# Kernel optimization log

Hardware: AMD Instinct MI355X
Metric: run time of the kernel (lower is better)

Reference implementation:

```python
import jax, jax.numpy as jnp
import numpy as np

B, N, S, C, NS = 2, 20000, 1024, 256, 16
RADIUS, HMIN, HMAX = 0.05, -0.02, 0.04
NA, ND = 12, 4
EPS = 1e-5  # BatchNorm eps


def setup_inputs() -> dict:
    key = jax.random.key(0)
    ks = jax.random.split(key, 40)
    def rn(k, shape, scale=0.05):
        return jax.random.normal(k, shape, jnp.float32) * scale
    inp = {
        "xyz": jax.random.uniform(ks[0], (B, N, 3), jnp.float32),
        "new_xyz": jax.random.uniform(ks[1], (B, S, 3), jnp.float32),
        "view_rot": jax.random.normal(ks[2], (B, S, 3, 3), jnp.float32),
        "features": jax.random.normal(ks[3], (B, C, N), jnp.float32),
    }
    i = 4
    for li, (o, ci) in enumerate([(512, C + 3), (256, 512), (256, 256)], 1):
        inp[f"mlp{li}_w"] = rn(ks[i], (o, ci)); inp[f"mlp{li}_b"] = rn(ks[i + 1], (o,))
        inp[f"mlp{li}_g"] = jnp.ones((o,), jnp.float32) + rn(ks[i + 2], (o,), 0.01)
        inp[f"mlp{li}_be"] = rn(ks[i + 3], (o,)); i += 4
    for name in ("c1", "c2"):
        inp[f"{name}_w"] = rn(ks[i], (256, 256)); inp[f"{name}_b"] = rn(ks[i + 1], (256,))
        inp[f"{name}_g"] = jnp.ones((256,), jnp.float32) + rn(ks[i + 2], (256,), 0.01)
        inp[f"{name}_be"] = rn(ks[i + 3], (256,)); i += 4
    inp["c3_w"] = rn(ks[i], (NA * ND * 2, 256)); inp["c3_b"] = rn(ks[i + 1], (NA * ND * 2,))
    return inp


def _bn(x, g, be):  # eval-mode BatchNorm with running_mean=0, running_var=1
    return x * (g / jnp.sqrt(1.0 + EPS)) + be


def _forward(xyz, new_xyz, view_rot, features,
             mlp1_w, mlp1_b, mlp1_g, mlp1_be,
             mlp2_w, mlp2_b, mlp2_g, mlp2_be,
             mlp3_w, mlp3_b, mlp3_g, mlp3_be,
             c1_w, c1_b, c1_g, c1_be,
             c2_w, c2_b, c2_g, c2_be,
             c3_w, c3_b):
    # ---- cylinder query (CUDA kernel math: r = rot @ (p - c), cylinder axis = x) ----
    # computed per rotation row to keep intermediates at (B,S,N) each
    comp = []
    for i in range(3):
        rw = view_rot[:, :, i, :]  # (B,S,3)
        comp.append(jnp.einsum('bsj,bpj->bsp', rw, xyz) - jnp.sum(rw * new_xyz, -1)[..., None])
    xr, yr, zr = comp  # each (B,S,N)
    mask = (yr * yr + zr * zr < RADIUS * RADIUS) & (xr > HMIN) & (xr < HMAX)
    # first-NS valid indices per seed (ascending), pad with first valid (0 if none)
    vals = jnp.where(mask, jnp.arange(N, dtype=jnp.int32), N)  # (B,S,N)
    neg_top, _ = jax.lax.top_k(-vals, NS)
    idx = -neg_top  # (B,S,NS) ascending
    first = idx[..., :1]
    first = jnp.where(first >= N, 0, first)
    idx = jnp.where(idx >= N, first, idx)
    # ---- group ----
    b_ix = jnp.arange(B)[:, None, None]
    g_xyz = xyz[b_ix, idx]                                  # (B,S,NS,3)
    g_feat = jnp.transpose(features, (0, 2, 1))[b_ix, idx]  # (B,S,NS,C)
    diff = (g_xyz - new_xyz[:, :, None, :]) / RADIUS        # normalize_xyz
    rot_xyz = jnp.einsum('bsnk,bskj->bsnj', diff, view_rot)  # rotate_xyz: diff @ rot
    h = jnp.concatenate([rot_xyz, g_feat], axis=-1)          # (B,S,NS,C+3)
    # ---- SharedMLP (1x1 conv2d + BN + ReLU) ----
    for w, bb, g, be in ((mlp1_w, mlp1_b, mlp1_g, mlp1_be),
                         (mlp2_w, mlp2_b, mlp2_g, mlp2_be),
                         (mlp3_w, mlp3_b, mlp3_g, mlp3_be)):
        h = jax.nn.relu(_bn(jnp.einsum('bsnc,oc->bsno', h, w) + bb, g, be))
    h = h.max(axis=2)  # max-pool over samples -> (B,S,256)
    # ---- pointwise conv1d head ----
    h = jax.nn.relu(_bn(jnp.einsum('bsc,oc->bso', h, c1_w) + c1_b, c1_g, c1_be))
    h = jax.nn.relu(_bn(jnp.einsum('bsc,oc->bso', h, c2_w) + c2_b, c2_g, c2_be))
    out = jnp.einsum('bsc,oc->bso', h, c3_w) + c3_b  # (B,S,NA*ND*2)
    return out


def reference(xyz, new_xyz, view_rot, features,
              mlp1_w, mlp1_b, mlp1_g, mlp1_be,
              mlp2_w, mlp2_b, mlp2_g, mlp2_be,
              mlp3_w, mlp3_b, mlp3_g, mlp3_be,
              c1_w, c1_b, c1_g, c1_be,
              c2_w, c2_b, c2_g, c2_be,
              c3_w, c3_b):
    return _forward(xyz, new_xyz, view_rot, features,
                    mlp1_w, mlp1_b, mlp1_g, mlp1_be,
                    mlp2_w, mlp2_b, mlp2_g, mlp2_be,
                    mlp3_w, mlp3_b, mlp3_g, mlp3_be,
                    c1_w, c1_b, c1_g, c1_be,
                    c2_w, c2_b, c2_g, c2_be,
                    c3_w, c3_b)
```

## Files before the change

kernel.cpp:

```cpp
#include <hip/hip_runtime.h>
#include <hip/hip_bf16.h>
#include <stdint.h>

#define B_   2
#define N_   20000
#define S_   1024
#define C_   256
#define NS_  16
#define NQ   (B_ * S_)
#define M_   (NQ * NS_)
#define K1P  288
#define O1   512
#define O2   256
#define O3   256
#define OUTC 96

#define R2C   ((float)(0.05 * 0.05))
#define HMINC ((float)(-0.02))
#define HMAXC ((float)(0.04))

__device__ __forceinline__ unsigned short f2b(float f) {
    union { float f; unsigned int i; } x; x.f = f;
    unsigned int r = x.i + 0x7FFFu + ((x.i >> 16) & 1u);
    return (unsigned short)(r >> 16);
}
__device__ __forceinline__ float b2f(unsigned short u) {
    union { unsigned int i; float f; } x; x.i = ((unsigned int)u) << 16; return x.f;
}

__global__ __launch_bounds__(256) void prep_w123(const float* __restrict__ m1w,
                                                 const float* __restrict__ m2w,
                                                 const float* __restrict__ m3w,
                                                 unsigned short* __restrict__ w1p,
                                                 unsigned short* __restrict__ w2p,
                                                 unsigned short* __restrict__ w3p) {
    int i = blockIdx.x * 256 + threadIdx.x;
    if (i < O1 * K1P) {
        int o = i / K1P, k = i - o * K1P;
        float v = 0.0f;
        if (k < 256)      v = m1w[o * 259 + 3 + k];
        else if (k < 259) v = m1w[o * 259 + (k - 256)];
        w1p[i] = (k < 259) ? f2b(v) : (unsigned short)0;
    } else if (i < O1 * K1P + O2 * 512) {
        int j = i - O1 * K1P;
        w2p[j] = f2b(m2w[j]);
    } else if (i < O1 * K1P + O2 * 512 + O3 * 256) {
        int j = i - O1 * K1P - O2 * 512;
        w3p[j] = f2b(m3w[j]);
    }
}

__global__ __launch_bounds__(256) void prep_head_w(const float* __restrict__ c1w,
                                                   const float* __restrict__ c2w,
                                                   const float* __restrict__ c3w,
                                                   unsigned short* __restrict__ c1wb,
                                                   unsigned short* __restrict__ c2wb,
                                                   unsigned short* __restrict__ c3wb) {
    int i = blockIdx.x * 256 + threadIdx.x;
    if (i < 65536) {
        c1wb[i] = f2b(c1w[i]);
    } else if (i < 131072) {
        c2wb[i - 65536] = f2b(c2w[i - 65536]);
    } else if (i < 163840) {
        int j = i - 131072;
        int o = j >> 8, k = j & 255;
        c3wb[j] = (o < OUTC) ? f2b(c3w[o * 256 + k]) : (unsigned short)0;
    }
}

__global__ __launch_bounds__(256) void transpose_feat(const float* __restrict__ feat,
                                                      unsigned short* __restrict__ feat_t) {
    __shared__ float tile[32][33];
    int n0 = blockIdx.x * 32, c0 = blockIdx.y * 32, b = blockIdx.z;
    int t = threadIdx.x;
    int nl = t & 31;
#pragma unroll
    for (int i = 0; i < 4; ++i) {
        int cl = (t >> 5) + i * 8;
        tile[cl][nl] = feat[((size_t)(b * C_ + c0 + cl)) * N_ + n0 + nl];
    }
    __syncthreads();
    int nr = t >> 3, c4 = (t & 7) * 4;
    ushort4 v;
    v.x = f2b(tile[c4 + 0][nr]);
    v.y = f2b(tile[c4 + 1][nr]);
    v.z = f2b(tile[c4 + 2][nr]);
    v.w = f2b(tile[c4 + 3][nr]);
    *(ushort4*)(feat_t + ((size_t)(b * N_ + n0 + nr)) * C_ + c0 + c4) = v;
}

__global__ __launch_bounds__(256) void cyl_query(const float* __restrict__ xyz,
                                                 const float* __restrict__ new_xyz,
                                                 const float* __restrict__ view_rot,
                                                 int* __restrict__ idx_out) {
#pragma clang fp contract(off)
    int q = blockIdx.x;
    int b = q >> 10;
    int t = threadIdx.x;
    int w = t >> 6, lane = t & 63;

    __shared__ int lists[4][NS_];
    __shared__ int cnts[4];

    const float* nq = new_xyz + (size_t)q * 3;
    float qx = nq[0], qy = nq[1], qz = nq[2];
    const float* rp = view_rot + (size_t)q * 9;
    float R[9];
#pragma unroll
    for (int i = 0; i < 9; ++i) R[i] = rp[i];
    float dq0 = (R[0]*qx + R[1]*qy) + R[2]*qz;
    float dq1 = (R[3]*qx + R[4]*qy) + R[5]*qz;
    float dq2 = (R[6]*qx + R[7]*qy) + R[8]*qz;

    int start = w * 5000;
    int end   = min(N_, start + 5000);
    int cnt = 0;
    const float* xb = xyz + (size_t)b * N_ * 3;

    for (int base = start; base < end && cnt < NS_; base += 64) {
        int p = base + lane;
        bool m = false;
        if (p < end) {
            const float* pp = xb + (size_t)p * 3;
            float px = pp[0], py = pp[1], pz = pp[2];
            float xr = ((R[0]*px + R[1]*py) + R[2]*pz) - dq0;
            float yr = ((R[3]*px + R[4]*py) + R[5]*pz) - dq1;
            float zr = ((R[6]*px + R[7]*py) + R[8]*pz) - dq2;
            m = ((yr*yr + zr*zr) < R2C) && (xr > HMINC) && (xr < HMAXC);
        }
        unsigned long long bal = __ballot(m);
        int below = __popcll(bal & ((1ull << lane) - 1ull));
        if (m) {
            int pos = cnt + below;
            if (pos < NS_) lists[w][pos] = p;
        }
        cnt += (int)__popcll(bal);
        if (cnt > NS_) cnt = NS_;
    }
    if (lane == 0) cnts[w] = cnt;
    __syncthreads();

    if (t == 0) {
        int buf[NS_]; int total = 0;
        for (int ww = 0; ww < 4 && total < NS_; ++ww)
            for (int i = 0; i < cnts[ww] && total < NS_; ++i)
                buf[total++] = lists[ww][i];
        int first = (total > 0) ? buf[0] : 0;
        for (int i = 0; i < NS_; ++i)
            idx_out[q * NS_ + i] = (i < total) ? buf[i] : first;
    }
}

__global__ __launch_bounds__(256) void build_h0(const float* __restrict__ xyz,
                                                const float* __restrict__ new_xyz,
                                                const float* __restrict__ view_rot,
                                                const unsigned short* __restrict__ feat_t,
                                                const int* __restrict__ idxs,
                                                unsigned short* __restrict__ h0) {
#pragma clang fp contract(off)
    int q = blockIdx.x;
    int b = q >> 10;
    int t = threadIdx.x;
    __shared__ int pidx[NS_];
    if (t < NS_) pidx[t] = idxs[q * NS_ + t];
    __syncthreads();

#pragma unroll
    for (int pass = 0; pass < 2; ++pass) {
        int n = pass * 8 + (t >> 5);
        int p = pidx[n];
        uint4 v = *(const uint4*)(feat_t + ((size_t)(b * N_ + p)) * C_ + (t & 31) * 8);
        *(uint4*)(h0 + (size_t)(q * NS_ + n) * K1P + (t & 31) * 8) = v;
    }

    if (t < NS_) {
        int n = t, p = pidx[n];
        const float* pp = xyz + ((size_t)b * N_ + p) * 3;
        const float* nq = new_xyz + (size_t)q * 3;
        float dx = (pp[0] - nq[0]) / 0.05f;
        float dy = (pp[1] - nq[1]) / 0.05f;
        float dz = (pp[2] - nq[2]) / 0.05f;
        const float* rp = view_rot + (size_t)q * 9;
        float r0 = (dx * rp[0] + dy * rp[3]) + dz * rp[6];
        float r1 = (dx * rp[1] + dy * rp[4]) + dz * rp[7];
        float r2 = (dx * rp[2] + dy * rp[5]) + dz * rp[8];
        size_t row = (size_t)(q * NS_ + n) * K1P;
        h0[row + 256] = f2b(r0);
        h0[row + 257] = f2b(r1);
        h0[row + 258] = f2b(r2);
    }
    for (int e = t; e < NS_ * 29; e += 256) {
        int n = e / 29, c = 259 + (e - n * 29);
        h0[(size_t)(q * NS_ + n) * K1P + c] = 0;
    }
}

typedef float f32x4 __attribute__((ext_vector_type(4)));
typedef short s16x8 __attribute__((ext_vector_type(8)));

__global__ __launch_bounds__(256) void gemm_bn_relu(const unsigned short* __restrict__ A,
                                                    const unsigned short* __restrict__ W,
                                                    const float* __restrict__ bias,
                                                    const float* __restrict__ gam,
                                                    const float* __restrict__ bet,
                                                    unsigned short* __restrict__ out,
                                                    int M, int Nn, int K) {
    __shared__ __align__(16) unsigned short As[128 * 32];
    __shared__ __align__(16) unsigned short Bs[128 * 32];
    int tid  = threadIdx.x;
    int lane = tid & 63, wave = tid >> 6;
    int m0 = blockIdx.x * 128, n0 = blockIdx.y * 128;
    int wm = (wave >> 1) * 64, wn = (wave & 1) * 64;

    f32x4 acc[4][4] = {};

    for (int k0 = 0; k0 < K; k0 += 32) {
        __syncthreads();
#pragma unroll
        for (int j = 0; j < 2; ++j) {
            int e = j * 256 + tid;
            int r = e >> 2, c8 = (e & 3) << 3;
            *(uint4*)&As[e * 8] = *(const uint4*)(A + (size_t)(m0 + r) * K + k0 + c8);
            *(uint4*)&Bs[e * 8] = *(const uint4*)(W + (size_t)(n0 + r) * K + k0 + c8);
        }
        __syncthreads();

        int kq = (lane >> 4) * 8, rr = lane & 15;
        s16x8 af[4], bfr[4];
#pragma unroll
        for (int i = 0; i < 4; ++i) af[i]  = *(const s16x8*)&As[(wm + i * 16 + rr) * 32 + kq];
#pragma unroll
        for (int j = 0; j < 4; ++j) bfr[j] = *(const s16x8*)&Bs[(wn + j * 16 + rr) * 32 + kq];
#pragma unroll
        for (int i = 0; i < 4; ++i)
#pragma unroll
            for (int j = 0; j < 4; ++j)
                acc[i][j] = __builtin_amdgcn_mfma_f32_16x16x32_bf16(af[i], bfr[j], acc[i][j], 0, 0, 0);
    }

    float inv = 1.0f / sqrtf(1.0f + 1e-5f);
    int col = lane & 15, rq = (lane >> 4) * 4;
#pragma unroll
    for (int j = 0; j < 4; ++j) {
        int n = n0 + wn + j * 16 + col;
        float sc = gam[n] * inv;
        float tb = bias[n] * sc + bet[n];
#pragma unroll
        for (int i = 0; i < 4; ++i) {
            int mbase = m0 + wm + i * 16 + rq;
#pragma unroll
            for (int r = 0; r < 4; ++r) {
                float v = acc[i][j][r] * sc + tb;
                v = fmaxf(v, 0.0f);
                out[(size_t)(mbase + r) * Nn + n] = f2b(v);
            }
        }
    }
}

__global__ __launch_bounds__(256) void gemm_bn_relu_maxpool(const unsigned short* __restrict__ A,
                                                            const unsigned short* __restrict__ W,
                                                            const float* __restrict__ bias,
                                                            const float* __restrict__ gam,
                                                            const float* __restrict__ bet,
                                                            unsigned short* __restrict__ hp,
                                                            int M, int Nn, int K) {
    __shared__ __align__(16) unsigned short As[128 * 32];
    __shared__ __align__(16) unsigned short Bs[128 * 32];
    int tid  = threadIdx.x;
    int lane = tid & 63, wave = tid >> 6;
    int m0 = blockIdx.x * 128, n0 = blockIdx.y * 128;
    int wm = (wave >> 1) * 64, wn = (wave & 1) * 64;

    f32x4 acc[4][4] = {};

    for (int k0 = 0; k0 < K; k0 += 32) {
        __syncthreads();
#pragma unroll
        for (int j = 0; j < 2; ++j) {
            int e = j * 256 + tid;
            int r = e >> 2, c8 = (e & 3) << 3;
            *(uint4*)&As[e * 8] = *(const uint4*)(A + (size_t)(m0 + r) * K + k0 + c8);
            *(uint4*)&Bs[e * 8] = *(const uint4*)(W + (size_t)(n0 + r) * K + k0 + c8);
        }
        __syncthreads();

        int kq = (lane >> 4) * 8, rr = lane & 15;
        s16x8 af[4], bfr[4];
#pragma unroll
        for (int i = 0; i < 4; ++i) af[i]  = *(const s16x8*)&As[(wm + i * 16 + rr) * 32 + kq];
#pragma unroll
        for (int j = 0; j < 4; ++j) bfr[j] = *(const s16x8*)&Bs[(wn + j * 16 + rr) * 32 + kq];
#pragma unroll
        for (int i = 0; i < 4; ++i)
#pragma unroll
            for (int j = 0; j < 4; ++j)
                acc[i][j] = __builtin_amdgcn_mfma_f32_16x16x32_bf16(af[i], bfr[j], acc[i][j], 0, 0, 0);
    }

    float inv = 1.0f / sqrtf(1.0f + 1e-5f);
    int col = lane & 15;
    int qbase = (m0 + wm) >> 4;
#pragma unroll
    for (int j = 0; j < 4; ++j) {
        int n = n0 + wn + j * 16 + col;
        float sc = gam[n] * inv;
        float tb = bias[n] * sc + bet[n];
#pragma unroll
        for (int i = 0; i < 4; ++i) {
            float mx = 0.0f;
#pragma unroll
            for (int r = 0; r < 4; ++r)
                mx = fmaxf(mx, acc[i][j][r] * sc + tb);
            mx = fmaxf(mx, __shfl_xor(mx, 16, 64));
            mx = fmaxf(mx, __shfl_xor(mx, 32, 64));
            if (lane < 16)
                hp[(size_t)(qbase + i) * Nn + n] = f2b(mx);
        }
    }
}

__global__ __launch_bounds__(256) void gemm_c3(const unsigned short* __restrict__ A,
                                               const unsigned short* __restrict__ W,
                                               const float* __restrict__ bias,
                                               float* __restrict__ out,
                                               int M, int K) {
    __shared__ __align__(16) unsigned short As[128 * 32];
    __shared__ __align__(16) unsigned short Bs[128 * 32];
    int tid  = threadIdx.x;
    int lane = tid & 63, wave = tid >> 6;
    int m0 = blockIdx.x * 128;
    int wm = (wave >> 1) * 64, wn = (wave & 1) * 64;

    f32x4 acc[4][4] = {};

    for (int k0 = 0; k0 < K; k0 += 32) {
        __syncthreads();
#pragma unroll
        for (int j = 0; j < 2; ++j) {
            int e = j * 256 + tid;
            int r = e >> 2, c8 = (e & 3) << 3;
            *(uint4*)&As[e * 8] = *(const uint4*)(A + (size_t)(m0 + r) * K + k0 + c8);
            *(uint4*)&Bs[e * 8] = *(const uint4*)(W + (size_t)r * K + k0 + c8);
        }
        __syncthreads();

        int kq = (lane >> 4) * 8, rr = lane & 15;
        s16x8 af[4], bfr[4];
#pragma unroll
        for (int i = 0; i < 4; ++i) af[i]  = *(const s16x8*)&As[(wm + i * 16 + rr) * 32 + kq];
#pragma unroll
        for (int j = 0; j < 4; ++j) bfr[j] = *(const s16x8*)&Bs[(wn + j * 16 + rr) * 32 + kq];
#pragma unroll
        for (int i = 0; i < 4; ++i)
#pragma unroll
            for (int j = 0; j < 4; ++j)
                acc[i][j] = __builtin_amdgcn_mfma_f32_16x16x32_bf16(af[i], bfr[j], acc[i][j], 0, 0, 0);
    }

    int col = lane & 15, rq = (lane >> 4) * 4;
#pragma unroll
    for (int j = 0; j < 4; ++j) {
        int n = wn + j * 16 + col;
        if (n >= OUTC) continue;
        float bb = bias[n];
#pragma unroll
        for (int i = 0; i < 4; ++i) {
            int mbase = m0 + wm + i * 16 + rq;
#pragma unroll
            for (int r = 0; r < 4; ++r)
                out[(size_t)(mbase + r) * OUTC + n] = acc[i][j][r] + bb;
        }
    }
}

extern "C" void kernel_launch(void* const* d_in, const int* in_sizes, int n_in,
                              void* d_out, int out_size, void* d_ws, size_t ws_size,
                              hipStream_t stream) {
    const float* xyz      = (const float*)d_in[0];
    const float* new_xyz  = (const float*)d_in[1];
    const float* view_rot = (const float*)d_in[2];
    const float* feat     = (const float*)d_in[3];
    const float* m1w = (const float*)d_in[4];
    const float* m1b = (const float*)d_in[5];
    const float* m1g = (const float*)d_in[6];
    const float* m1be= (const float*)d_in[7];
    const float* m2w = (const float*)d_in[8];
    const float* m2b = (const float*)d_in[9];
    const float* m2g = (const float*)d_in[10];
    const float* m2be= (const float*)d_in[11];
    const float* m3w = (const float*)d_in[12];
    const float* m3b = (const float*)d_in[13];
    const float* m3g = (const float*)d_in[14];
    const float* m3be= (const float*)d_in[15];
    const float* c1w = (const float*)d_in[16];
    const float* c1b = (const float*)d_in[17];
    const float* c1g = (const float*)d_in[18];
    const float* c1be= (const float*)d_in[19];
    const float* c2w = (const float*)d_in[20];
    const float* c2b = (const float*)d_in[21];
    const float* c2g = (const float*)d_in[22];
    const float* c2be= (const float*)d_in[23];
    const float* c3w = (const float*)d_in[24];
    const float* c3b = (const float*)d_in[25];

    char* ws = (char*)d_ws;
    int*            idxs = (int*)ws;
    unsigned short* w1p  = (unsigned short*)(ws + 131072);
    unsigned short* w2p  = (unsigned short*)(ws + 425984);
    unsigned short* w3p  = (unsigned short*)(ws + 688128);
    unsigned short* h0   = (unsigned short*)(ws + 819200);
    char*           h1b  = ws + 19693568;
    unsigned short* h1   = (unsigned short*)h1b;
    unsigned short* h2   = h0;
    unsigned short* featt= (unsigned short*)(h1b + 12582912);
    unsigned short* hp   = (unsigned short*)(h1b + 0);
    unsigned short* g1   = (unsigned short*)(h1b + 4194304);
    unsigned short* g2   = (unsigned short*)(h1b + 8388608);
    unsigned short* c1wb = (unsigned short*)(h1b + 12582912);
    unsigned short* c2wb = (unsigned short*)(h1b + 13631488);
    unsigned short* c3wb = (unsigned short*)(h1b + 14680064);

    hipLaunchKernelGGL(prep_w123, dim3((O1 * K1P + O2 * 512 + O3 * 256) / 256), dim3(256), 0, stream,
                       m1w, m2w, m3w, w1p, w2p, w3p);
    hipLaunchKernelGGL(cyl_query, dim3(NQ), dim3(256), 0, stream, xyz, new_xyz, view_rot, idxs);
    hipLaunchKernelGGL(transpose_feat, dim3(N_ / 32, C_ / 32, B_), dim3(256), 0, stream, feat, featt);
    hipLaunchKernelGGL(build_h0, dim3(NQ), dim3(256), 0, stream, xyz, new_xyz, view_rot, featt, idxs, h0);
    hipLaunchKernelGGL(gemm_bn_relu, dim3(M_ / 128, O1 / 128), dim3(256), 0, stream,
                       h0, w1p, m1b, m1g, m1be, h1, M_, O1, K1P);
    hipLaunchKernelGGL(gemm_bn_relu, dim3(M_ / 128, O2 / 128), dim3(256), 0, stream,
                       h1, w2p, m2b, m2g, m2be, h2, M_, O2, 512);
    hipLaunchKernelGGL(prep_head_w, dim3(163840 / 256), dim3(256), 0, stream,
                       c1w, c2w, c3w, c1wb, c2wb, c3wb);
    hipLaunchKernelGGL(gemm_bn_relu_maxpool, dim3(M_ / 128, O3 / 128), dim3(256), 0, stream,
                       h2, w3p, m3b, m3g, m3be, hp, M_, O3, 256);
    hipLaunchKernelGGL(gemm_bn_relu, dim3(NQ / 128, 256 / 128), dim3(256), 0, stream,
                       hp, c1wb, c1b, c1g, c1be, g1, NQ, 256, 256);
    hipLaunchKernelGGL(gemm_bn_relu, dim3(NQ / 128, 256 / 128), dim3(256), 0, stream,
                       g1, c2wb, c2b, c2g, c2be, g2, NQ, 256, 256);
    hipLaunchKernelGGL(gemm_c3, dim3(NQ / 128), dim3(256), 0, stream,
                       g2, c3wb, c3b, (float*)d_out, NQ, 256);
}
```

Measured before the change: 266.0 us.

## Replace brute-force cylinder query with uniform grid spatial hashing

Points are bucketed into a 16^3 uniform grid per batch using count, scan and scatter kernels. Each query then scans only the cells overlapping a conservative bounding box of its cylinder, computed from the inverse rotation. Candidates are kept in a per-wave shared buffer, and a wave-level selection picks the 16 smallest indices, which preserves the reference ordering. This is meant to cut the O(N) scan per query, at the cost of four extra small launches and atomics. The saving shrinks if the inverse rotations make the boxes large.

```diff
diff --git a/kernel.cpp b/kernel.cpp
--- a/kernel.cpp
+++ b/kernel.cpp
@@ -1,6 +1,7 @@
 #include <hip/hip_runtime.h>
 #include <hip/hip_bf16.h>
 #include <stdint.h>
+#include <limits.h>
 
 #define B_   2
 #define N_   20000
@@ -18,6 +19,11 @@
 #define R2C   ((float)(0.05 * 0.05))
 #define HMINC ((float)(-0.02))
 #define HMAXC ((float)(0.04))
+
+#define GDIM   16
+#define GCELLS (GDIM * GDIM * GDIM)
+#define GTOT   (B_ * GCELLS)
+#define CAP    256
 
 __device__ __forceinline__ unsigned short f2b(float f) {
     union { float f; unsigned int i; } x; x.f = f;
@@ -89,18 +95,112 @@
     *(ushort4*)(feat_t + ((size_t)(b * N_ + n0 + nr)) * C_ + c0 + c4) = v;
 }
 
-__global__ __launch_bounds__(256) void cyl_query(const float* __restrict__ xyz,
-                                                 const float* __restrict__ new_xyz,
-                                                 const float* __restrict__ view_rot,
-                                                 int* __restrict__ idx_out) {
+__global__ __launch_bounds__(256) void grid_zero(int* __restrict__ c) {
+    c[blockIdx.x * 256 + threadIdx.x] = 0;
+}
+
+__device__ __forceinline__ int cell_of(float px, float py, float pz, int b) {
+    int cx = (int)(px * (float)GDIM); cx = min(GDIM - 1, max(0, cx));
+    int cy = (int)(py * (float)GDIM); cy = min(GDIM - 1, max(0, cy));
+    int cz = (int)(pz * (float)GDIM); cz = min(GDIM - 1, max(0, cz));
+    return b * GCELLS + cz * (GDIM * GDIM) + cy * GDIM + cx;
+}
+
+__global__ __launch_bounds__(256) void grid_count(const float* __restrict__ xyz,
+                                                  int* __restrict__ counts) {
+    int i = blockIdx.x * 256 + threadIdx.x;
+    if (i < B_ * N_) {
+        int b = i / N_;
+        const float* p = xyz + (size_t)i * 3;
+        atomicAdd(counts + cell_of(p[0], p[1], p[2], b), 1);
+    }
+}
+
+__global__ __launch_bounds__(256) void grid_scan(const int* __restrict__ counts,
+                                                 int* __restrict__ start,
+                                                 int* __restrict__ cursor) {
+    __shared__ int part[256];
+    int t = threadIdx.x;
+    int local[32];
+    int s = 0;
+#pragma unroll
+    for (int i = 0; i < 32; ++i) { local[i] = counts[t * 32 + i]; s += local[i]; }
+    part[t] = s;
+    __syncthreads();
+    if (t == 0) {
+        int r = 0;
+        for (int i = 0; i < 256; ++i) { int x = part[i]; part[i] = r; r += x; }
+    }
+    __syncthreads();
+    int r = part[t];
+#pragma unroll
+    for (int i = 0; i < 32; ++i) {
+        start[t * 32 + i] = r;
+        cursor[t * 32 + i] = r;
+        r += local[i];
+    }
+    if (t == 255) start[GTOT] = r;
+}
+
+__global__ __launch_bounds__(256) void grid_scatter(const float* __restrict__ xyz,
+                                                    int* __restrict__ cursor,
+                                                    float4* __restrict__ sorted) {
+    int i = blockIdx.x * 256 + threadIdx.x;
+    if (i < B_ * N_) {
+        int b = i / N_, n = i - b * N_;
+        const float* p = xyz + (size_t)i * 3;
+        float px = p[0], py = p[1], pz = p[2];
+        int pos = atomicAdd(cursor + cell_of(px, py, pz, b), 1);
+        sorted[pos] = make_float4(px, py, pz, __int_as_float(n));
+    }
+}
+
+__device__ __forceinline__ void sort16(int* buf, int cnt, int lane) {
+    asm volatile("s_waitcnt lgkmcnt(0)" ::: "memory");
+    __builtin_amdgcn_sched_barrier(0);
+    int a0 = INT_MAX, a1 = INT_MAX, a2 = INT_MAX, a3 = INT_MAX;
+    if (lane < cnt)       a0 = buf[lane];
+    if (lane + 64 < cnt)  a1 = buf[lane + 64];
+    if (lane + 128 < cnt) a2 = buf[lane + 128];
+    if (lane + 192 < cnt) a3 = buf[lane + 192];
+#pragma unroll
+    for (int t = 0; t < NS_; ++t) {
+        int v = a0, sl = 0;
+        if (a1 < v) { v = a1; sl = 1; }
+        if (a2 < v) { v = a2; sl = 2; }
+        if (a3 < v) { v = a3; sl = 3; }
+        int pp = (sl << 6) | lane;
+#pragma unroll
+        for (int off = 1; off < 64; off <<= 1) {
+            int ov = __shfl_xor(v, off);
+            int op = __shfl_xor(pp, off);
+            if (ov < v) { v = ov; pp = op; }
+        }
+        if ((pp & 63) == lane) {
+            int s = pp >> 6;
+            if (s == 0) a0 = INT_MAX;
+            else if (s == 1) a1 = INT_MAX;
+            else if (s == 2) a2 = INT_MAX;
+            else a3 = INT_MAX;
+        }
+        if (lane == 0) buf[t] = v;
+    }
+    asm volatile("s_waitcnt lgkmcnt(0)" ::: "memory");
+    __builtin_amdgcn_sched_barrier(0);
+}
+
+__global__ __launch_bounds__(256) void cyl_query_grid(const float* __restrict__ new_xyz,
+                                                      const float* __restrict__ view_rot,
+                                                      const float4* __restrict__ sorted,
+                                                      const int* __restrict__ cell_start,
+                                                      int* __restrict__ idx_out) {
 #pragma clang fp contract(off)
-    int q = blockIdx.x;
+    int w = threadIdx.x >> 6, lane = threadIdx.x & 63;
+    int q = blockIdx.x * 4 + w;
     int b = q >> 10;
-    int t = threadIdx.x;
-    int w = t >> 6, lane = t & 63;
-
-    __shared__ int lists[4][NS_];
-    __shared__ int cnts[4];
+
+    __shared__ int bufs[4][CAP];
+    int* buf = bufs[w];
 
     const float* nq = new_xyz + (size_t)q * 3;
     float qx = nq[0], qy = nq[1], qz = nq[2];
@@ -112,42 +212,76 @@
     float dq1 = (R[3]*qx + R[4]*qy) + R[5]*qz;
     float dq2 = (R[6]*qx + R[7]*qy) + R[8]*qz;
 
-    int start = w * 5000;
-    int end   = min(N_, start + 5000);
-    int cnt = 0;
-    const float* xb = xyz + (size_t)b * N_ * 3;
-
-    for (int base = start; base < end && cnt < NS_; base += 64) {
-        int p = base + lane;
-        bool m = false;
-        if (p < end) {
-            const float* pp = xb + (size_t)p * 3;
-            float px = pp[0], py = pp[1], pz = pp[2];
-            float xr = ((R[0]*px + R[1]*py) + R[2]*pz) - dq0;
-            float yr = ((R[3]*px + R[4]*py) + R[5]*pz) - dq1;
-            float zr = ((R[6]*px + R[7]*py) + R[8]*pz) - dq2;
-            m = ((yr*yr + zr*zr) < R2C) && (xr > HMINC) && (xr < HMAXC);
-        }
-        unsigned long long bal = __ballot(m);
-        int below = __popcll(bal & ((1ull << lane) - 1ull));
-        if (m) {
-            int pos = cnt + below;
-            if (pos < NS_) lists[w][pos] = p;
-        }
-        cnt += (int)__popcll(bal);
-        if (cnt > NS_) cnt = NS_;
-    }
-    if (lane == 0) cnts[w] = cnt;
-    __syncthreads();
-
-    if (t == 0) {
-        int buf[NS_]; int total = 0;
-        for (int ww = 0; ww < 4 && total < NS_; ++ww)
-            for (int i = 0; i < cnts[ww] && total < NS_; ++i)
-                buf[total++] = lists[ww][i];
-        int first = (total > 0) ? buf[0] : 0;
-        for (int i = 0; i < NS_; ++i)
-            idx_out[q * NS_ + i] = (i < total) ? buf[i] : first;
+    int x0 = 0, x1 = GDIM - 1, y0 = 0, y1 = GDIM - 1, z0 = 0, z1 = GDIM - 1;
+    {
+        float det = R[0]*(R[4]*R[8]-R[5]*R[7])
+                  - R[1]*(R[3]*R[8]-R[5]*R[6])
+                  + R[2]*(R[3]*R[7]-R[4]*R[6]);
+        float adet = fabsf(det);
+        if (adet > 1e-30f) {
+            float id = 1.0f / det;
+            float m00 = (R[4]*R[8]-R[5]*R[7])*id, m01 = (R[2]*R[7]-R[1]*R[8])*id, m02 = (R[1]*R[5]-R[2]*R[4])*id;
+            float m10 = (R[5]*R[6]-R[3]*R[8])*id, m11 = (R[0]*R[8]-R[2]*R[6])*id, m12 = (R[2]*R[3]-R[0]*R[5])*id;
+            float m20 = (R[3]*R[7]-R[4]*R[6])*id, m21 = (R[1]*R[6]-R[0]*R[7])*id, m22 = (R[0]*R[4]-R[1]*R[3])*id;
+            const float mid = 0.5f * (HMINC + HMAXC);
+            const float hh  = 0.5f * (HMAXC - HMINC);
+            float cx = qx + m00 * mid, cy = qy + m10 * mid, cz = qz + m20 * mid;
+            float ex = hh * fabsf(m00) + 0.05f * sqrtf(m01*m01 + m02*m02);
+            float ey = hh * fabsf(m10) + 0.05f * sqrtf(m11*m11 + m12*m12);
+            float ez = hh * fabsf(m20) + 0.05f * sqrtf(m21*m21 + m22*m22);
+            ex = ex * 1.002f + 1e-3f;
+            ey = ey * 1.002f + 1e-3f;
+            ez = ez * 1.002f + 1e-3f;
+            x0 = (int)fmaxf(0.0f, fminf((float)(GDIM - 1), floorf((cx - ex) * (float)GDIM)));
+            x1 = (int)fmaxf(0.0f, fminf((float)(GDIM - 1), floorf((cx + ex) * (float)GDIM)));
+            y0 = (int)fmaxf(0.0f, fminf((float)(GDIM - 1), floorf((cy - ey) * (float)GDIM)));
+            y1 = (int)fmaxf(0.0f, fminf((float)(GDIM - 1), floorf((cy + ey) * (float)GDIM)));
+            z0 = (int)fmaxf(0.0f, fminf((float)(GDIM - 1), floorf((cz - ez) * (float)GDIM)));
+            z1 = (int)fmaxf(0.0f, fminf((float)(GDIM - 1), floorf((cz + ez) * (float)GDIM)));
+        }
+    }
+
+    int cnt = 0, tot = 0;
+    int cbase = b * GCELLS;
+    for (int zc = z0; zc <= z1; ++zc) {
+        for (int yc = y0; yc <= y1; ++yc) {
+            int cid = cbase + zc * (GDIM * GDIM) + yc * GDIM;
+            int s = cell_start[cid + x0];
+            int e = cell_start[cid + x1 + 1];
+            for (int base = s; base < e; base += 64) {
+                int p = base + lane;
+                bool m = false;
+                int n = 0;
+                if (p < e) {
+                    float4 v = sorted[p];
+                    n = __float_as_int(v.w);
+                    float px = v.x, py = v.y, pz = v.z;
+                    float xr = ((R[0]*px + R[1]*py) + R[2]*pz) - dq0;
+                    float yr = ((R[3]*px + R[4]*py) + R[5]*pz) - dq1;
+                    float zr = ((R[6]*px + R[7]*py) + R[8]*pz) - dq2;
+                    m = ((yr*yr + zr*zr) < R2C) && (xr > HMINC) && (xr < HMAXC);
+                }
+                unsigned long long bal = __ballot(m);
+                if (m) {
+                    int pos = cnt + __popcll(bal & ((1ull << lane) - 1ull));
+                    buf[pos] = n;
+                }
+                int h = __popcll(bal);
+                cnt += h; tot += h;
+                if (cnt > CAP - 64) {
+                    sort16(buf, cnt, lane);
+                    cnt = NS_;
+                }
+            }
+        }
+    }
+
+    sort16(buf, cnt, lane);
+    int total = tot < NS_ ? tot : NS_;
+    if (lane < NS_) {
+        int first = (tot > 0) ? buf[0] : 0;
+        int v = (lane < total) ? buf[lane] : first;
+        idx_out[q * NS_ + lane] = v;
     }
 }
 
@@ -420,10 +554,19 @@
     unsigned short* c1wb = (unsigned short*)(h1b + 12582912);
     unsigned short* c2wb = (unsigned short*)(h1b + 13631488);
     unsigned short* c3wb = (unsigned short*)(h1b + 14680064);
+    float4*         srt  = (float4*)(h1b + 0);
+    int*            gcnt = (int*)(h1b + 640000);
+    int*            gsta = (int*)(h1b + 672768);
+    int*            gcur = (int*)(h1b + 705552);
 
     hipLaunchKernelGGL(prep_w123, dim3((O1 * K1P + O2 * 512 + O3 * 256) / 256), dim3(256), 0, stream,
                        m1w, m2w, m3w, w1p, w2p, w3p);
-    hipLaunchKernelGGL(cyl_query, dim3(NQ), dim3(256), 0, stream, xyz, new_xyz, view_rot, idxs);
+    hipLaunchKernelGGL(grid_zero, dim3(GTOT / 256), dim3(256), 0, stream, gcnt);
+    hipLaunchKernelGGL(grid_count, dim3((B_ * N_ + 255) / 256), dim3(256), 0, stream, xyz, gcnt);
+    hipLaunchKernelGGL(grid_scan, dim3(1), dim3(256), 0, stream, gcnt, gsta, gcur);
+    hipLaunchKernelGGL(grid_scatter, dim3((B_ * N_ + 255) / 256), dim3(256), 0, stream, xyz, gcur, srt);
+    hipLaunchKernelGGL(cyl_query_grid, dim3(NQ / 4), dim3(256), 0, stream,
+                       new_xyz, view_rot, srt, gsta, idxs);
     hipLaunchKernelGGL(transpose_feat, dim3(N_ / 32, C_ / 32, B_), dim3(256), 0, stream, feat, featt);
     hipLaunchKernelGGL(build_h0, dim3(NQ), dim3(256), 0, stream, xyz, new_xyz, view_rot, featt, idxs, h0);
     hipLaunchKernelGGL(gemm_bn_relu, dim3(M_ / 128, O1 / 128), dim3(256), 0, stream,
```

Measured after the change: 401.2 us. 1.51x slower.
